# Optimization experiments

Measured on AMD Instinct MI355X. Metric: run time of the kernel, lower is better.

Reference implementation:

```python
import jax, jax.numpy as jnp
import numpy as np

N = 2048
NONGT = 2048
EMB = 64
GROUP = 16
FEAT = 256
DM = 1024  # dim[0] == dim[1]
DHEAD = DM // GROUP  # 64


def setup_inputs() -> dict:
    key = jax.random.key(0)
    ks = jax.random.split(key, 12)
    s = lambda fan_in: 1.0 / np.sqrt(fan_in)
    return {
        "roi_feat": jax.random.normal(ks[0], (N, FEAT), jnp.float32),
        "position_embedding": jax.random.uniform(ks[1], (N, NONGT, EMB), jnp.float32),
        "fc1_w": jax.random.normal(ks[2], (GROUP, EMB), jnp.float32) * s(EMB),
        "fc1_b": jnp.zeros((GROUP,), jnp.float32),
        "fc2_w": jax.random.normal(ks[3], (DM, FEAT), jnp.float32) * s(FEAT),
        "fc2_b": jnp.zeros((DM,), jnp.float32),
        "fc3_w": jax.random.normal(ks[4], (DM, FEAT), jnp.float32) * s(FEAT),
        "fc3_b": jnp.zeros((DM,), jnp.float32),
        "conv_w": jax.random.normal(ks[5], (FEAT, GROUP * FEAT), jnp.float32) * s(GROUP * FEAT),
        "conv_b": jnp.zeros((FEAT,), jnp.float32),
        "nongt_dim": NONGT,
    }


def reference(roi_feat, position_embedding, fc1_w, fc1_b, fc2_w, fc2_b,
              fc3_w, fc3_b, conv_w, conv_b, nongt_dim):
    nongt_roi_feat = roi_feat[:nongt_dim, :]                      # [M, FEAT]
    # position bias: relu(fc1(pe)) -> [N, M, G] -> [N, G, M]
    pos1 = jax.nn.relu(jnp.einsum('nme,ge->nmg', position_embedding, fc1_w) + fc1_b)
    aff_weight = jnp.transpose(pos1, (0, 2, 1))                   # [N, G, M]
    # grouped Q, K
    q = roi_feat @ fc2_w.T + fc2_b                                # [N, DM]
    q = q.reshape(-1, GROUP, DHEAD)                               # [N, G, d]
    k = nongt_roi_feat @ fc3_w.T + fc3_b                          # [M, DM]
    k = k.reshape(-1, GROUP, DHEAD)                               # [M, G, d]
    scale = 1.0 / np.sqrt(float(DHEAD))
    aff = jnp.einsum('ngd,mgd->ngm', q, k) * scale                # [N, G, M]
    weighted = jnp.log(jnp.maximum(aff_weight, 1e-6)) + aff
    aff_softmax = jax.nn.softmax(weighted, axis=-1)               # [N, G, M]
    out_t = jnp.einsum('ngm,mc->ngc', aff_softmax, nongt_roi_feat)  # [N, G, FEAT]
    flat = out_t.reshape(out_t.shape[0], GROUP * FEAT)            # channel order g*FEAT + c
    return flat @ conv_w.T + conv_b                               # [N, FEAT]
```

## Files before the change

kernel.cpp:

```cpp
#include <hip/hip_runtime.h>
#include <hip/hip_bf16.h>

#define NQ   2048
#define NK   2048
#define EMB  64
#define GRP  16
#define FEAT 256

typedef __bf16 bf16x8 __attribute__((ext_vector_type(8)));
typedef __bf16 bf16x4 __attribute__((ext_vector_type(4)));
typedef float  f32x4  __attribute__((ext_vector_type(4)));

#define MFMA(a, b, c) __builtin_amdgcn_mfma_f32_16x16x32_bf16((a), (b), (c), 0, 0, 0)

typedef __attribute__((address_space(3))) unsigned int  lds_u32;
typedef __attribute__((address_space(1))) unsigned int  glb_u32;

static __device__ __forceinline__ bf16x8 cvt8(float4 a, float4 b) {
    bf16x8 r;
    r[0] = (__bf16)a.x; r[1] = (__bf16)a.y; r[2] = (__bf16)a.z; r[3] = (__bf16)a.w;
    r[4] = (__bf16)b.x; r[5] = (__bf16)b.y; r[6] = (__bf16)b.z; r[7] = (__bf16)b.w;
    return r;
}

__global__ void prep_roiT(const float* __restrict__ roi, __bf16* __restrict__ roiT) {
    __shared__ float tile[64][65];
    const int tid = threadIdx.x;
    const int m0 = (blockIdx.x >> 2) * 64, c0 = (blockIdx.x & 3) * 64;
    const int tr = tid >> 4, tc = tid & 15;
#pragma unroll
    for (int ch = 0; ch < 4; ++ch) {
        int r = ch * 16 + tr;
        float4 v = *(const float4*)(roi + (m0 + r) * 256 + c0 + tc * 4);
        tile[r][tc * 4 + 0] = v.x; tile[r][tc * 4 + 1] = v.y;
        tile[r][tc * 4 + 2] = v.z; tile[r][tc * 4 + 3] = v.w;
    }
    __syncthreads();
#pragma unroll
    for (int ch = 0; ch < 4; ++ch) {
        int crow = ch * 16 + tr;
        int mm = tc * 4;
        bf16x4 o;
        o[0] = (__bf16)tile[mm + 0][crow]; o[1] = (__bf16)tile[mm + 1][crow];
        o[2] = (__bf16)tile[mm + 2][crow]; o[3] = (__bf16)tile[mm + 3][crow];
        *(bf16x4*)(roiT + (c0 + crow) * 2048 + m0 + mm) = o;
    }
}

__global__ void prep_cast(const float* __restrict__ in, __bf16* __restrict__ out, int n4) {
    int idx = blockIdx.x * blockDim.x + threadIdx.x;
    for (int i = idx; i < n4; i += gridDim.x * blockDim.x) {
        float4 v = ((const float4*)in)[i];
        bf16x4 o;
        o[0] = (__bf16)v.x; o[1] = (__bf16)v.y; o[2] = (__bf16)v.z; o[3] = (__bf16)v.w;
        ((bf16x4*)out)[i] = o;
    }
}

__global__ void prep_qk(const float* __restrict__ roi,
                        const float* __restrict__ Wq, const float* __restrict__ bq,
                        const float* __restrict__ Wk, const float* __restrict__ bk,
                        __bf16* __restrict__ outq, __bf16* __restrict__ outk) {
    const float* W    = blockIdx.y ? Wk   : Wq;
    const float* bias = blockIdx.y ? bk   : bq;
    __bf16*      out  = blockIdx.y ? outk : outq;
    const int tid = threadIdx.x, l = tid & 63, wid = tid >> 6;
    const int n0 = (blockIdx.x >> 2) * 16;
    const int dmB = (blockIdx.x & 3) * 256 + wid * 64;
    const int lr = l & 15, lk = l >> 4;
    f32x4 acc[4];
#pragma unroll
    for (int i = 0; i < 4; ++i) acc[i] = (f32x4){0.f, 0.f, 0.f, 0.f};
    for (int k0 = 0; k0 < 256; k0 += 32) {
        const float* ap = roi + (n0 + lr) * 256 + k0 + lk * 8;
        bf16x8 af = cvt8(*(const float4*)ap, *(const float4*)(ap + 4));
#pragma unroll
        for (int cf = 0; cf < 4; ++cf) {
            const float* bp = W + (dmB + cf * 16 + lr) * 256 + k0 + lk * 8;
            acc[cf] = MFMA(af, cvt8(*(const float4*)bp, *(const float4*)(bp + 4)), acc[cf]);
        }
    }
#pragma unroll
    for (int cf = 0; cf < 4; ++cf) {
        int dm = dmB + cf * 16 + lr;
        float bv = bias[dm];
        int g = dm >> 6, d = dm & 63;
#pragma unroll
        for (int ri = 0; ri < 4; ++ri) {
            int n = n0 + lk * 4 + ri;
            out[(g * 2048 + n) * 64 + d] = (__bf16)(acc[cf][ri] + bv);
        }
    }
}

__launch_bounds__(256, 4)
__global__ void w_gemm(const float* __restrict__ pe,
                       const float* __restrict__ fc1w,
                       const float* __restrict__ fc1b,
                       __bf16* __restrict__ wg) {
    const int tid = threadIdx.x, l = tid & 63, wid = tid >> 6;
    const int lr = l & 15, lk = l >> 4;
    const long n = blockIdx.x >> 2;
    const int mbase = (blockIdx.x & 3) * 512 + wid * 128;

    bf16x8 fcB[2];
#pragma unroll
    for (int s = 0; s < 2; ++s) {
        const float* p = fc1w + lr * 64 + s * 32 + lk * 8;
        fcB[s] = cvt8(*(const float4*)p, *(const float4*)(p + 4));
    }
    const float bias = fc1b[lr];

    const float* pebase = pe + (n * 2048 + mbase + lr) * 64 + lk * 8;
    __bf16* obase = wg + (n * 16 + lr) * 2048 + mbase + lk * 4;

#pragma unroll 4
    for (int it = 0; it < 8; ++it) {
        const float* p0 = pebase + it * 16 * 64;
        f32x4 c = (f32x4){0.f, 0.f, 0.f, 0.f};
        c = MFMA(cvt8(*(const float4*)(p0),      *(const float4*)(p0 + 4)),  fcB[0], c);
        c = MFMA(cvt8(*(const float4*)(p0 + 32), *(const float4*)(p0 + 36)), fcB[1], c);
        bf16x4 o;
#pragma unroll
        for (int ri = 0; ri < 4; ++ri)
            o[ri] = (__bf16)fmaxf(fmaxf(c[ri] + bias, 0.f), 1e-6f);
        *(bf16x4*)(obase + it * 16) = o;
    }
}

#define P_BASE 32768
__launch_bounds__(512, 2)
__global__ void relation_attn(const __bf16* __restrict__ wg,
                              const __bf16* __restrict__ qb,
                              const __bf16* __restrict__ kb,
                              const __bf16* __restrict__ roiT,
                              __bf16* __restrict__ flat) {
    __shared__ __align__(16) unsigned char smem[49152];
    const int tid = threadIdx.x;
    const int l   = tid & 63;
    const int wid = tid >> 6;
    const int n0  = blockIdx.x * 8;
    const int lr  = l & 15;
    const int lk  = l >> 4;
    const int gh  = lk >> 1;
    const int nqh = lk & 1;
    const int g2  = wid * 2;
    const int gA  = g2 + gh;

    bf16x8 qa[2][2];
#pragma unroll
    for (int gi = 0; gi < 2; ++gi)
#pragma unroll
        for (int s = 0; s < 2; ++s)
            qa[gi][s] = *(const bf16x8*)(qb + (long)((g2 + gi) * 2048 + n0 + (lr & 7)) * 64 + s * 32 + lk * 8);

    f32x4 acc[16];
#pragma unroll
    for (int i = 0; i < 16; ++i) acc[i] = (f32x4){0.f, 0.f, 0.f, 0.f};
    float dsum[4] = {0.f, 0.f, 0.f, 0.f};

    const __bf16* wptr = wg + (long)((n0 + (nqh << 2)) * 16 + gA) * 2048 + lr;

    for (int t = 0; t < 32; ++t) {
        const int m0t = t * 64;
        __syncthreads();

        {
            const int crow = l >> 3, slot = l & 7;
#pragma unroll
            for (int i = 0; i < 4; ++i) {
                int c = wid * 32 + i * 8 + crow;
                int D = slot ^ (c & 7);
                const __bf16* gp = roiT + c * 2048 + m0t + D * 8;
                __builtin_amdgcn_global_load_lds(
                    (const glb_u32*)(const void*)gp,
                    (lds_u32*)(void*)(smem + wid * 4096 + i * 1024), 16, 0, 0);
            }
        }

        float wlv[4][4];
#pragma unroll
        for (int mf = 0; mf < 4; ++mf)
#pragma unroll
            for (int ri = 0; ri < 4; ++ri)
                wlv[mf][ri] = (float)wptr[(long)ri * 32768 + m0t + mf * 16];

        f32x4 a0[4], a1[4];
#pragma unroll
        for (int mf = 0; mf < 4; ++mf) {
            const __bf16* kp = kb + (long)(g2 * 2048 + m0t + mf * 16 + lr) * 64 + lk * 8;
            bf16x8 k0 = *(const bf16x8*)(kp);
            bf16x8 k1 = *(const bf16x8*)(kp + 32);
            f32x4 z = (f32x4){0.f, 0.f, 0.f, 0.f};
            z = MFMA(qa[0][0], k0, z);
            z = MFMA(qa[0][1], k1, z);
            a0[mf] = z;
        }
#pragma unroll
        for (int mf = 0; mf < 4; ++mf) {
            const __bf16* kp = kb + (long)((g2 + 1) * 2048 + m0t + mf * 16 + lr) * 64 + lk * 8;
            bf16x8 k0 = *(const bf16x8*)(kp);
            bf16x8 k1 = *(const bf16x8*)(kp + 32);
            f32x4 z = (f32x4){0.f, 0.f, 0.f, 0.f};
            z = MFMA(qa[1][0], k0, z);
            z = MFMA(qa[1][1], k1, z);
            a1[mf] = z;
        }

#pragma unroll
        for (int mf = 0; mf < 4; ++mf) {
            int mm = mf * 16 + lr;
#pragma unroll
            for (int ri = 0; ri < 4; ++ri) {
                float a = gh ? a1[mf][ri] : a0[mf][ri];
                int n2 = (nqh << 2) + ri;
                float pv = wlv[mf][ri] * __expf(a * 0.125f);
                dsum[ri] += pv;
                int rp = (gA << 3) + n2;
                int poff = (rp << 7) + ((mm ^ (n2 << 3)) << 1);
                *(__bf16*)(smem + P_BASE + poff) = (__bf16)pv;
            }
        }

        __syncthreads();

        {
            const int rpA = wid * 16 + lr;
            const int QA = (rpA & 7) << 3;
#pragma unroll
            for (int s = 0; s < 2; ++s) {
                bf16x8 pA = *(const bf16x8*)(smem + P_BASE + (rpA << 7)
                                             + (((s * 32 + lk * 8) ^ QA) << 1));
#pragma unroll
                for (int cf = 0; cf < 16; ++cf) {
                    int c = cf * 16 + lr;
                    bf16x8 rB = *(const bf16x8*)(smem + c * 128
                                                 + (((s * 4 + lk) ^ (c & 7)) << 4));
                    acc[cf] = MFMA(pA, rB, acc[cf]);
                }
            }
        }
    }

    float inv[4];
#pragma unroll
    for (int ri = 0; ri < 4; ++ri) {
        float v = dsum[ri];
        v += __shfl_xor(v, 1); v += __shfl_xor(v, 2);
        v += __shfl_xor(v, 4); v += __shfl_xor(v, 8);
        inv[ri] = 1.0f / v;
    }
#pragma unroll
    for (int cf = 0; cf < 16; ++cf) {
        int c = cf * 16 + lr;
#pragma unroll
        for (int ri = 0; ri < 4; ++ri) {
            int n2 = (nqh << 2) + ri;
            flat[(long)(n0 + n2) * 4096 + gA * 256 + c] = (__bf16)(acc[cf][ri] * inv[ri]);
        }
    }
}

__launch_bounds__(256)
__global__ void conv_gemm(const __bf16* __restrict__ flat, const __bf16* __restrict__ cw,
                          const float* __restrict__ cb, float* __restrict__ out) {
    const int tid = threadIdx.x, l = tid & 63, wid = tid >> 6;
    const int n0 = (blockIdx.x >> 1) * 16;
    const int j0 = (blockIdx.x & 1) * 128 + wid * 32;
    const int lr = l & 15, lk = l >> 4;
    f32x4 acc[2] = {(f32x4){0.f, 0.f, 0.f, 0.f}, (f32x4){0.f, 0.f, 0.f, 0.f}};
#pragma unroll 4
    for (int k0 = 0; k0 < 4096; k0 += 32) {
        bf16x8 af = *(const bf16x8*)(flat + (long)(n0 + lr) * 4096 + k0 + lk * 8);
#pragma unroll
        for (int cf = 0; cf < 2; ++cf) {
            bf16x8 bfr = *(const bf16x8*)(cw + (long)(j0 + cf * 16 + lr) * 4096 + k0 + lk * 8);
            acc[cf] = MFMA(af, bfr, acc[cf]);
        }
    }
#pragma unroll
    for (int cf = 0; cf < 2; ++cf) {
        int j = j0 + cf * 16 + lr;
        float bv = cb[j];
#pragma unroll
        for (int ri = 0; ri < 4; ++ri)
            out[(n0 + lk * 4 + ri) * 256 + j] = acc[cf][ri] + bv;
    }
}

extern "C" void kernel_launch(void* const* d_in, const int* in_sizes, int n_in,
                              void* d_out, int out_size, void* d_ws, size_t ws_size,
                              hipStream_t stream) {
    const float* roi  = (const float*)d_in[0];
    const float* pe   = (const float*)d_in[1];
    const float* fc1w = (const float*)d_in[2];
    const float* fc1b = (const float*)d_in[3];
    const float* fc2w = (const float*)d_in[4];
    const float* fc2b = (const float*)d_in[5];
    const float* fc3w = (const float*)d_in[6];
    const float* fc3b = (const float*)d_in[7];
    const float* cw   = (const float*)d_in[8];
    const float* cb   = (const float*)d_in[9];
    float* out = (float*)d_out;

    unsigned char* ws = (unsigned char*)d_ws;
    __bf16* roiT   = (__bf16*)(ws);
    __bf16* convwb = (__bf16*)(ws + (1ull  << 20));
    __bf16* qb     = (__bf16*)(ws + (3ull  << 20));
    __bf16* kb     = (__bf16*)(ws + (7ull  << 20));
    __bf16* flat   = (__bf16*)(ws + (11ull << 20));
    __bf16* wg     = (__bf16*)(ws + (27ull << 20));

    w_gemm<<<8192, 256, 0, stream>>>(pe, fc1w, fc1b, wg);
    prep_roiT<<<128, 256, 0, stream>>>(roi, roiT);
    prep_cast<<<512, 256, 0, stream>>>(cw, convwb, (256 * 4096) / 4);
    prep_qk<<<dim3(512, 2), 256, 0, stream>>>(roi, fc2w, fc2b, fc3w, fc3b, qb, kb);
    relation_attn<<<256, 512, 0, stream>>>(wg, qb, kb, roiT, flat);
    conv_gemm<<<256, 256, 0, stream>>>(flat, convwb, cb, out);
}
```

Before: 514.9 us.

## Fuse position-embedding fc1 projection into the relation attention kernel

Removes the separate w_gemm kernel and its bf16 intermediate tensor of shape [N,16,2048]. Each attention tile now computes relu(fc1(pe)) on the fly with MFMA, stages the result in a swizzled shared-memory region, and reads it back per group. This cuts the global write and re-read of the weight tensor and one launch. In exchange it adds LDS use (64 KB per block), an extra __syncthreads per tile, and puts the large position-embedding stream inside the attention loop, where it may stall compute.

Measured after the change: 535.5 us. 1.04x slower.

```diff
diff --git a/kernel.cpp b/kernel.cpp
--- a/kernel.cpp
+++ b/kernel.cpp
@@ -93,49 +93,17 @@
     }
 }
 
-__launch_bounds__(256, 4)
-__global__ void w_gemm(const float* __restrict__ pe,
-                       const float* __restrict__ fc1w,
-                       const float* __restrict__ fc1b,
-                       __bf16* __restrict__ wg) {
-    const int tid = threadIdx.x, l = tid & 63, wid = tid >> 6;
-    const int lr = l & 15, lk = l >> 4;
-    const long n = blockIdx.x >> 2;
-    const int mbase = (blockIdx.x & 3) * 512 + wid * 128;
-
-    bf16x8 fcB[2];
-#pragma unroll
-    for (int s = 0; s < 2; ++s) {
-        const float* p = fc1w + lr * 64 + s * 32 + lk * 8;
-        fcB[s] = cvt8(*(const float4*)p, *(const float4*)(p + 4));
-    }
-    const float bias = fc1b[lr];
-
-    const float* pebase = pe + (n * 2048 + mbase + lr) * 64 + lk * 8;
-    __bf16* obase = wg + (n * 16 + lr) * 2048 + mbase + lk * 4;
-
-#pragma unroll 4
-    for (int it = 0; it < 8; ++it) {
-        const float* p0 = pebase + it * 16 * 64;
-        f32x4 c = (f32x4){0.f, 0.f, 0.f, 0.f};
-        c = MFMA(cvt8(*(const float4*)(p0),      *(const float4*)(p0 + 4)),  fcB[0], c);
-        c = MFMA(cvt8(*(const float4*)(p0 + 32), *(const float4*)(p0 + 36)), fcB[1], c);
-        bf16x4 o;
-#pragma unroll
-        for (int ri = 0; ri < 4; ++ri)
-            o[ri] = (__bf16)fmaxf(fmaxf(c[ri] + bias, 0.f), 1e-6f);
-        *(bf16x4*)(obase + it * 16) = o;
-    }
-}
-
 #define P_BASE 32768
+#define W_BASE 49152
 __launch_bounds__(512, 2)
-__global__ void relation_attn(const __bf16* __restrict__ wg,
+__global__ void relation_attn(const float* __restrict__ pe,
+                              const float* __restrict__ fc1w,
+                              const float* __restrict__ fc1b,
                               const __bf16* __restrict__ qb,
                               const __bf16* __restrict__ kb,
                               const __bf16* __restrict__ roiT,
                               __bf16* __restrict__ flat) {
-    __shared__ __align__(16) unsigned char smem[49152];
+    __shared__ __align__(16) unsigned char smem[65536];
     const int tid = threadIdx.x;
     const int l   = tid & 63;
     const int wid = tid >> 6;
@@ -154,12 +122,19 @@
         for (int s = 0; s < 2; ++s)
             qa[gi][s] = *(const bf16x8*)(qb + (long)((g2 + gi) * 2048 + n0 + (lr & 7)) * 64 + s * 32 + lk * 8);
 
+    bf16x8 fcB[2];
+#pragma unroll
+    for (int s = 0; s < 2; ++s) {
+        const float* p = fc1w + lr * 64 + s * 32 + lk * 8;
+        fcB[s] = cvt8(*(const float4*)p, *(const float4*)(p + 4));
+    }
+    const float wbias = fc1b[lr];
+    const float* pebase = pe + ((long)(n0 + wid) * 2048) * 64 + lk * 8;
+
     f32x4 acc[16];
 #pragma unroll
     for (int i = 0; i < 16; ++i) acc[i] = (f32x4){0.f, 0.f, 0.f, 0.f};
     float dsum[4] = {0.f, 0.f, 0.f, 0.f};
-
-    const __bf16* wptr = wg + (long)((n0 + (nqh << 2)) * 16 + gA) * 2048 + lr;
 
     for (int t = 0; t < 32; ++t) {
         const int m0t = t * 64;
@@ -178,12 +153,24 @@
             }
         }
 
-        float wlv[4][4];
-#pragma unroll
-        for (int mf = 0; mf < 4; ++mf)
-#pragma unroll
-            for (int ri = 0; ri < 4; ++ri)
-                wlv[mf][ri] = (float)wptr[(long)ri * 32768 + m0t + mf * 16];
+        {
+            const float* pt = pebase + (long)m0t * 64;
+#pragma unroll
+            for (int mf = 0; mf < 4; ++mf) {
+                const float* pr = pt + (mf * 16 + lr) * 64;
+                f32x4 wa = (f32x4){0.f, 0.f, 0.f, 0.f};
+                wa = MFMA(cvt8(*(const float4*)(pr),      *(const float4*)(pr + 4)),  fcB[0], wa);
+                wa = MFMA(cvt8(*(const float4*)(pr + 32), *(const float4*)(pr + 36)), fcB[1], wa);
+                bf16x4 o;
+#pragma unroll
+                for (int ri = 0; ri < 4; ++ri)
+                    o[ri] = (__bf16)fmaxf(fmaxf(wa[ri] + wbias, 0.f), 1e-6f);
+                int woff = W_BASE + wid * 2048 + lr * 128
+                         + (((((mf << 1) + (lk >> 1)) ^ (lr & 7))) << 4)
+                         + ((lk & 1) << 3);
+                *(bf16x4*)(smem + woff) = o;
+            }
+        }
 
         f32x4 a0[4], a1[4];
 #pragma unroll
@@ -207,14 +194,19 @@
             a1[mf] = z;
         }
 
+        __syncthreads();
+
 #pragma unroll
         for (int mf = 0; mf < 4; ++mf) {
             int mm = mf * 16 + lr;
+            int xs = ((((mf << 1) + (lr >> 3)) ^ (gA & 7)) << 4);
+            const unsigned char* wrow = smem + W_BASE + gA * 128 + xs + ((mm & 7) << 1);
 #pragma unroll
             for (int ri = 0; ri < 4; ++ri) {
+                int n2 = (nqh << 2) + ri;
+                float wv = (float)*(const __bf16*)(wrow + n2 * 2048);
                 float a = gh ? a1[mf][ri] : a0[mf][ri];
-                int n2 = (nqh << 2) + ri;
-                float pv = wlv[mf][ri] * __expf(a * 0.125f);
+                float pv = wv * __expf(a * 0.125f);
                 dsum[ri] += pv;
                 int rp = (gA << 3) + n2;
                 int poff = (rp << 7) + ((mm ^ (n2 << 3)) << 1);
@@ -309,12 +301,10 @@
     __bf16* qb     = (__bf16*)(ws + (3ull  << 20));
     __bf16* kb     = (__bf16*)(ws + (7ull  << 20));
     __bf16* flat   = (__bf16*)(ws + (11ull << 20));
-    __bf16* wg     = (__bf16*)(ws + (27ull << 20));
-
-    w_gemm<<<8192, 256, 0, stream>>>(pe, fc1w, fc1b, wg);
+
     prep_roiT<<<128, 256, 0, stream>>>(roi, roiT);
     prep_cast<<<512, 256, 0, stream>>>(cw, convwb, (256 * 4096) / 4);
     prep_qk<<<dim3(512, 2), 256, 0, stream>>>(roi, fc2w, fc2b, fc3w, fc3b, qb, kb);
-    relation_attn<<<256, 512, 0, stream>>>(wg, qb, kb, roiT, flat);
+    relation_attn<<<256, 512, 0, stream>>>(pe, fc1w, fc1b, qb, kb, roiT, flat);
     conv_gemm<<<256, 256, 0, stream>>>(flat, convwb, cb, out);
 }
```
